# Optimization experiments

Hardware: AMD Instinct MI355X
Metric: run time of the kernel (lower is better)

Reference implementation:

```python
import jax, jax.numpy as jnp
import numpy as np

B, C, H, W = 8, 256, 132, 132
NH = 8          # num_head
WIN = 6         # pooled window (AdaptiveAvgPool2d output 6x6)


def setup_inputs() -> dict:
    key = jax.random.key(0)
    ks = jax.random.split(key, 16)
    def rn(k, shape, s=0.02):
        return jax.random.normal(k, shape, jnp.float32) * s
    d = {}
    d["x"] = jax.random.normal(ks[0], (B, C, H, W), jnp.float32)
    d["x_e"] = jax.random.normal(ks[1], (B, C, H, W), jnp.float32)
    # LayerNorms
    d["norm_w"] = jnp.ones((C,), jnp.float32); d["norm_b"] = jnp.zeros((C,), jnp.float32)
    d["norme_w"] = jnp.ones((C,), jnp.float32); d["norme_b"] = jnp.zeros((C,), jnp.float32)
    # GFA params (linears stored as (in, out))
    d["l_w"] = rn(ks[2], (C, C)); d["l_b"] = jnp.zeros((C,), jnp.float32)
    d["kv_w"] = rn(ks[3], (C, C)); d["kv_b"] = jnp.zeros((C,), jnp.float32)
    d["xe_w"] = rn(ks[4], (2 * C, C // 2)); d["xe_b"] = jnp.zeros((C // 2,), jnp.float32)
    # LFA params (single module, shared for both calls)
    d["q_w"] = rn(ks[5], (C, C // 2)); d["q_b"] = jnp.zeros((C // 2,), jnp.float32)
    d["ef_w"] = rn(ks[6], (C, C // 2)); d["ef_b"] = jnp.zeros((C // 2,), jnp.float32)
    d["ec_w"] = rn(ks[7], (C // 2, 1, 7, 7))   # depthwise 7x7, OIHW
    d["ec_b"] = jnp.zeros((C // 2,), jnp.float32)
    d["eb_w"] = rn(ks[8], (C // 2, C // 2)); d["eb_b"] = jnp.zeros((C // 2,), jnp.float32)
    # output projections (3C/2 -> C)
    d["proj_w"] = rn(ks[9], (3 * C // 2, C)); d["proj_b"] = jnp.zeros((C,), jnp.float32)
    d["proje_w"] = rn(ks[10], (3 * C // 2, C)); d["proje_b"] = jnp.zeros((C,), jnp.float32)
    return d


def _ln(x, w, b, eps=1e-6):
    m = x.mean(-1, keepdims=True)
    v = ((x - m) ** 2).mean(-1, keepdims=True)
    return (x - m) * jax.lax.rsqrt(v + eps) * w + b


def _gfa(x, xe, l_w, l_b, kv_w, kv_b, xe_w, xe_b):
    Bv, Hv, Wv, Cv = x.shape
    d = Cv // NH // 2                                   # per-head dim (=16)
    cat = jnp.concatenate([x, xe], -1)                  # (B,H,W,2C)
    xg = jax.nn.gelu(x @ l_w + l_b, approximate=False)  # nn.GELU exact
    kv = (xg @ kv_w + kv_b).reshape(Bv, Hv * Wv, 2, NH, d).transpose(2, 0, 3, 1, 4)
    k, v = kv[0], kv[1]                                 # (B,nh,HW,d)
    # AdaptiveAvgPool2d((6,6)) with H,W divisible by 6 == blocked mean
    pooled = cat.reshape(Bv, WIN, Hv // WIN, WIN, Wv // WIN, 2 * Cv).mean((2, 4))  # (B,6,6,2C)
    m = (pooled @ xe_w + xe_b).reshape(Bv, WIN * WIN, NH, d).transpose(0, 2, 1, 3)  # (B,nh,36,d)
    attn = jax.nn.softmax(jnp.einsum('bnqd,bnkd->bnqk', m * (d ** -0.5), k), axis=-1)
    out = jnp.einsum('bnqk,bnkd->bnqd', attn, v)        # (B,nh,36,d)
    out = out.reshape(Bv, NH, WIN, WIN, d).transpose(0, 1, 4, 2, 3).reshape(Bv, Cv // 2, WIN, WIN)
    up = jax.image.resize(out, (Bv, Cv // 2, Hv, Wv), 'bilinear')  # align_corners=False
    return up.transpose(0, 2, 3, 1)                     # (B,H,W,C/2)


def _lfa(x, xe, q_w, q_b, ef_w, ef_b, ec_w, ec_b, eb_w, eb_b):
    q = x @ q_w + q_b                                   # (B,H,W,C/2)
    e = (xe @ ef_w + ef_b).transpose(0, 3, 1, 2)        # (B,C/2,H,W)
    e = jax.lax.conv_general_dilated(
        e, ec_w, (1, 1), [(3, 3), (3, 3)],
        dimension_numbers=('NCHW', 'OIHW', 'NCHW'),
        feature_group_count=e.shape[1])
    e = (e + ec_b[None, :, None, None]).transpose(0, 2, 3, 1)
    e = e @ eb_w + eb_b
    return q * e


def reference(x, x_e, norm_w, norm_b, norme_w, norme_b,
              l_w, l_b, kv_w, kv_b, xe_w, xe_b,
              q_w, q_b, ef_w, ef_b, ec_w, ec_b, eb_w, eb_b,
              proj_w, proj_b, proje_w, proje_b):
    xc = x.transpose(0, 2, 3, 1)    # (B,H,W,C)
    xec = x_e.transpose(0, 2, 3, 1)
    xc = _ln(xc, norm_w, norm_b)
    xec = _ln(xec, norme_w, norme_b)
    g = _gfa(xc, xec, l_w, l_b, kv_w, kv_b, xe_w, xe_b)
    l1 = _lfa(xc, xec, q_w, q_b, ef_w, ef_b, ec_w, ec_b, eb_w, eb_b)
    l2 = _lfa(xec, xc, q_w, q_b, ef_w, ef_b, ec_w, ec_b, eb_w, eb_b)
    cat = jnp.concatenate([g, l1, l2], -1)              # (B,H,W,3C/2)
    out_e = (cat @ proje_w + proje_b).transpose(0, 3, 1, 2)
    out = (cat @ proj_w + proj_b).transpose(0, 3, 1, 2)
    return out, out_e
```

## Files before the change

### kernel.cpp

```cpp
#include <hip/hip_runtime.h>
#include <math.h>

#define HW_ 17424
#define WID 132
#define HGT 132
#define CH 256
#define MROWS 139392
#define OUTOFF 35684352

typedef __bf16 bf16x8 __attribute__((ext_vector_type(8)));
typedef float  f32x4  __attribute__((ext_vector_type(4)));

__device__ __forceinline__ void split8(const float* v, bf16x8& hi, bf16x8& lo) {
#pragma unroll
    for (int e = 0; e < 8; ++e) {
        float f = v[e];
        __bf16 h = (__bf16)f;
        hi[e] = h;
        lo[e] = (__bf16)(f - (float)h);
    }
}

__global__ __launch_bounds__(256)
void ln_k(const float* __restrict__ x, const float* __restrict__ w,
          const float* __restrict__ bias, float* __restrict__ out) {
    __shared__ float4 s1[256];
    __shared__ float4 s2[256];
    const int tid = threadIdx.x;
    const int b   = blockIdx.y;
    const int hw0 = blockIdx.x << 2;
    const float* px = x + ((size_t)(b * CH + tid)) * HW_ + hw0;
    float4 v = *(const float4*)px;
    s1[tid] = v;
    s2[tid] = make_float4(v.x * v.x, v.y * v.y, v.z * v.z, v.w * v.w);
    __syncthreads();
    for (int off = 128; off > 0; off >>= 1) {
        if (tid < off) {
            float4 a = s1[tid], c = s1[tid + off];
            a.x += c.x; a.y += c.y; a.z += c.z; a.w += c.w;
            s1[tid] = a;
            float4 d = s2[tid], e = s2[tid + off];
            d.x += e.x; d.y += e.y; d.z += e.z; d.w += e.w;
            s2[tid] = d;
        }
        __syncthreads();
    }
    float4 sum = s1[0], sq = s2[0];
    const float wv = w[tid], bv = bias[tid];
    const float inv = 1.0f / 256.0f;
    float o[4];
    {
        float m = sum.x * inv; float var = sq.x * inv - m * m;
        o[0] = (v.x - m) * rsqrtf(var + 1e-6f) * wv + bv;
    }
    {
        float m = sum.y * inv; float var = sq.y * inv - m * m;
        o[1] = (v.y - m) * rsqrtf(var + 1e-6f) * wv + bv;
    }
    {
        float m = sum.z * inv; float var = sq.z * inv - m * m;
        o[2] = (v.z - m) * rsqrtf(var + 1e-6f) * wv + bv;
    }
    {
        float m = sum.w * inv; float var = sq.w * inv - m * m;
        o[3] = (v.w - m) * rsqrtf(var + 1e-6f) * wv + bv;
    }
    float* po = out + ((size_t)(b * HW_ + hw0)) * CH + tid;
    po[0] = o[0]; po[256] = o[1]; po[512] = o[2]; po[768] = o[3];
}

template <int EPI, int KK, int NN>
__global__ __launch_bounds__(256, 2)
void mgemm_k(const float* __restrict__ A, const float* __restrict__ W,
             const float* __restrict__ bias, float* __restrict__ C,
             const float* __restrict__ mulbuf) {
    const int tid  = threadIdx.x;
    const int lane = tid & 63;
    const int wave = tid >> 6;
    const int wm = wave >> 1, wn = wave & 1;
    const int row0 = blockIdx.y * 128 + wm * 64;
    const int col0 = blockIdx.x * 128 + wn * 64;
    const int lrow = lane & 15;
    const int kg   = lane >> 4;

    const f32x4 zero = {0.f, 0.f, 0.f, 0.f};
    f32x4 acc[4][4];
#pragma unroll
    for (int i = 0; i < 4; ++i)
#pragma unroll
        for (int j = 0; j < 4; ++j) acc[i][j] = zero;

    for (int kt = 0; kt < KK; kt += 32) {
        const int kb = kt + kg * 8;
        bf16x8 ah[4], al[4], bh[4], bl[4];
#pragma unroll
        for (int mf = 0; mf < 4; ++mf) {
            const float* p = A + (size_t)(row0 + mf * 16 + lrow) * KK + kb;
            float buf[8];
            *(float4*)&buf[0] = *(const float4*)p;
            *(float4*)&buf[4] = *(const float4*)(p + 4);
            split8(buf, ah[mf], al[mf]);
        }
#pragma unroll
        for (int nf = 0; nf < 4; ++nf) {
            const float* p = W + (size_t)kb * NN + col0 + nf * 16 + lrow;
            float buf[8];
#pragma unroll
            for (int e = 0; e < 8; ++e) buf[e] = p[(size_t)e * NN];
            split8(buf, bh[nf], bl[nf]);
        }
#pragma unroll
        for (int mf = 0; mf < 4; ++mf)
#pragma unroll
            for (int nf = 0; nf < 4; ++nf) {
                f32x4 c = acc[mf][nf];
                c = __builtin_amdgcn_mfma_f32_16x16x32_bf16(al[mf], bh[nf], c, 0, 0, 0);
                c = __builtin_amdgcn_mfma_f32_16x16x32_bf16(ah[mf], bl[nf], c, 0, 0, 0);
                c = __builtin_amdgcn_mfma_f32_16x16x32_bf16(ah[mf], bh[nf], c, 0, 0, 0);
                acc[mf][nf] = c;
            }
    }

    float bv[4];
#pragma unroll
    for (int nf = 0; nf < 4; ++nf) bv[nf] = bias[col0 + nf * 16 + lrow];
#pragma unroll
    for (int mf = 0; mf < 4; ++mf) {
#pragma unroll
        for (int r = 0; r < 4; ++r) {
            const int row = row0 + mf * 16 + kg * 4 + r;
#pragma unroll
            for (int nf = 0; nf < 4; ++nf) {
                const int col = col0 + nf * 16 + lrow;
                const size_t off = (size_t)row * NN + col;
                float v = acc[mf][nf][r] + bv[nf];
                if (EPI == 1) v = 0.5f * v * (1.0f + erff(v * 0.7071067811865475f));
                if (EPI == 2) v *= mulbuf[off];
                C[off] = v;
            }
        }
    }
}

__global__ __launch_bounds__(256, 2)
void mgemm_proj_k(const float* __restrict__ g, const float* __restrict__ l1,
                  const float* __restrict__ l2,
                  const float* __restrict__ w1, const float* __restrict__ b1,
                  const float* __restrict__ w2, const float* __restrict__ b2,
                  float* __restrict__ out) {
    const int tid  = threadIdx.x;
    const int lane = tid & 63;
    const int wave = tid >> 6;
    const int wm = wave >> 1, wn = wave & 1;
    const int row0  = blockIdx.y * 128 + wm * 64;
    const int half  = blockIdx.x >> 1;
    const int ncol0 = (blockIdx.x & 1) * 128 + wn * 64;
    const float* Wsel = half ? w2 : w1;
    const float* bsel = half ? b2 : b1;
    float* obase = out + (half ? (size_t)OUTOFF : (size_t)0);
    const int lrow = lane & 15;
    const int kg   = lane >> 4;

    const f32x4 zero = {0.f, 0.f, 0.f, 0.f};
    f32x4 acc[4][4];
#pragma unroll
    for (int i = 0; i < 4; ++i)
#pragma unroll
        for (int j = 0; j < 4; ++j) acc[i][j] = zero;

    for (int kt = 0; kt < 384; kt += 32) {
        const float* Ab = (kt < 128) ? g : (kt < 256) ? l1 : l2;
        const int kloc = (kt & 127) + kg * 8;
        bf16x8 ah[4], al[4], bh[4], bl[4];
#pragma unroll
        for (int mf = 0; mf < 4; ++mf) {
            const float* p = Ab + (size_t)(row0 + mf * 16 + lrow) * 128 + kloc;
            float buf[8];
            *(float4*)&buf[0] = *(const float4*)p;
            *(float4*)&buf[4] = *(const float4*)(p + 4);
            split8(buf, ah[mf], al[mf]);
        }
#pragma unroll
        for (int nf = 0; nf < 4; ++nf) {
            const float* p = Wsel + (size_t)(kt + kg * 8) * 256 + ncol0 + nf * 16 + lrow;
            float buf[8];
#pragma unroll
            for (int e = 0; e < 8; ++e) buf[e] = p[(size_t)e * 256];
            split8(buf, bh[nf], bl[nf]);
        }
#pragma unroll
        for (int mf = 0; mf < 4; ++mf)
#pragma unroll
            for (int nf = 0; nf < 4; ++nf) {
                f32x4 c = acc[mf][nf];
                c = __builtin_amdgcn_mfma_f32_16x16x32_bf16(al[mf], bh[nf], c, 0, 0, 0);
                c = __builtin_amdgcn_mfma_f32_16x16x32_bf16(ah[mf], bl[nf], c, 0, 0, 0);
                c = __builtin_amdgcn_mfma_f32_16x16x32_bf16(ah[mf], bh[nf], c, 0, 0, 0);
                acc[mf][nf] = c;
            }
    }

    float bv[4];
#pragma unroll
    for (int nf = 0; nf < 4; ++nf) bv[nf] = bsel[ncol0 + nf * 16 + lrow];
#pragma unroll
    for (int mf = 0; mf < 4; ++mf) {
#pragma unroll
        for (int r = 0; r < 4; ++r) {
            const int row = row0 + mf * 16 + kg * 4 + r;
            const int bidx = row / HW_;
            const int hw = row - bidx * HW_;
#pragma unroll
            for (int nf = 0; nf < 4; ++nf) {
                const int c = ncol0 + nf * 16 + lrow;
                obase[((size_t)(bidx * 256 + c)) * HW_ + hw] = acc[mf][nf][r] + bv[nf];
            }
        }
    }
}

__global__ __launch_bounds__(256)
void pool_k(const float* __restrict__ xcl, const float* __restrict__ xel,
            float* __restrict__ pooled) {
    const int q = blockIdx.x;
    const int b = blockIdx.y;
    const int wi = q / 6, wj = q % 6;
    const int tid = threadIdx.x;
    const size_t base = ((size_t)(b * HW_ + wi * 22 * WID + wj * 22)) * CH + tid;
    const float* p0 = xcl + base;
    const float* p1 = xel + base;
    float s0 = 0.f, s1 = 0.f;
    for (int iy = 0; iy < 22; ++iy) {
        const size_t ro = (size_t)iy * WID * CH;
        for (int ix = 0; ix < 22; ++ix) {
            const size_t off = ro + (size_t)ix * CH;
            s0 += p0[off];
            s1 += p1[off];
        }
    }
    const float inv = 1.0f / 484.0f;
    float* dst = pooled + (size_t)(b * 36 + q) * 512;
    dst[tid] = s0 * inv;
    dst[256 + tid] = s1 * inv;
}

__global__ __launch_bounds__(128)
void mproj_k(const float* __restrict__ pooled, const float* __restrict__ xe_w,
             const float* __restrict__ xe_b, float* __restrict__ mbuf) {
    __shared__ float p[512];
    const int q = blockIdx.x, b = blockIdx.y, tid = threadIdx.x;
    const float* prow = pooled + (size_t)(b * 36 + q) * 512;
    for (int i = tid; i < 512; i += 128) p[i] = prow[i];
    __syncthreads();
    float acc = xe_b[tid];
    for (int k = 0; k < 512; ++k) acc += p[k] * xe_w[k * 128 + tid];
    mbuf[(size_t)(b * 36 + q) * 128 + tid] = acc;
}

__global__ __launch_bounds__(256)
void attn_k(const float* __restrict__ mbuf, const float* __restrict__ kv,
            float* __restrict__ aout) {
    const int qg = blockIdx.x;
    const int head = blockIdx.y, b = blockIdx.z;
    const int tid = threadIdx.x;
    __shared__ float ml[6][16];
    if (tid < 96) {
        const int q = tid >> 4, d = tid & 15;
        ml[q][d] = mbuf[(size_t)(b * 36 + qg * 6 + q) * 128 + head * 16 + d];
    }
    __syncthreads();

    float mx[6], sum[6], a[6][16];
#pragma unroll
    for (int q = 0; q < 6; ++q) {
        mx[q] = -INFINITY; sum[q] = 0.f;
#pragma unroll
        for (int d = 0; d < 16; ++d) a[q][d] = 0.f;
    }

    for (int j = tid; j < HW_; j += 256) {
        const float* row = kv + ((size_t)(b * HW_ + j)) * 256 + head * 16;
        float k[16], v[16];
        *(float4*)&k[0]  = *(const float4*)(row + 0);
        *(float4*)&k[4]  = *(const float4*)(row + 4);
        *(float4*)&k[8]  = *(const float4*)(row + 8);
        *(float4*)&k[12] = *(const float4*)(row + 12);
        const float* vr = row + 128;
        *(float4*)&v[0]  = *(const float4*)(vr + 0);
        *(float4*)&v[4]  = *(const float4*)(vr + 4);
        *(float4*)&v[8]  = *(const float4*)(vr + 8);
        *(float4*)&v[12] = *(const float4*)(vr + 12);
#pragma unroll
        for (int q = 0; q < 6; ++q) {
            float s = 0.f;
#pragma unroll
            for (int d = 0; d < 16; ++d) s += ml[q][d] * k[d];
            s *= 0.25f;
            const float nm = fmaxf(mx[q], s);
            const float corr = expf(mx[q] - nm);
            const float p = expf(s - nm);
            sum[q] = sum[q] * corr + p;
#pragma unroll
            for (int d = 0; d < 16; ++d) a[q][d] = a[q][d] * corr + p * v[d];
            mx[q] = nm;
        }
    }

    __shared__ float smax[256];
    __shared__ float ssum[256];
    __shared__ float sacc[256][16];
    for (int q = 0; q < 6; ++q) {
        __syncthreads();
        smax[tid] = mx[q]; ssum[tid] = sum[q];
#pragma unroll
        for (int d = 0; d < 16; ++d) sacc[tid][d] = a[q][d];
        for (int off = 128; off > 0; off >>= 1) {
            __syncthreads();
            if (tid < off) {
                const float ma = smax[tid], mb = smax[tid + off];
                const float nm = fmaxf(ma, mb);
                const float ea = expf(ma - nm), eb = expf(mb - nm);
                ssum[tid] = ssum[tid] * ea + ssum[tid + off] * eb;
                for (int d = 0; d < 16; ++d)
                    sacc[tid][d] = sacc[tid][d] * ea + sacc[tid + off][d] * eb;
                smax[tid] = nm;
            }
        }
        __syncthreads();
        if (tid < 16)
            aout[((size_t)(b * 8 + head) * 36 + qg * 6 + q) * 16 + tid] =
                sacc[0][tid] / ssum[0];
    }
}

__global__ __launch_bounds__(256)
void upsample_k(const float* __restrict__ aout, float* __restrict__ g) {
    const int tid = threadIdx.x;
    const int c = tid & 127;
    const int hw = blockIdx.x * 2 + (tid >> 7);
    const int b = blockIdx.y;
    const int h = hw / WID;
    const int w = hw - h * WID;
    const float fy = (h - 10.5f) * (1.0f / 22.0f);
    const float fx = (w - 10.5f) * (1.0f / 22.0f);
    float y0f = floorf(fy), x0f = floorf(fx);
    const float ty = fy - y0f, tx = fx - x0f;
    int y0 = (int)y0f, x0 = (int)x0f;
    int y1 = min(y0 + 1, 5), x1 = min(x0 + 1, 5);
    y0 = max(y0, 0); x0 = max(x0, 0);
    const int head = c >> 4, di = c & 15;
    const float* src = aout + ((size_t)(b * 8 + head) * 36) * 16 + di;
    const float s00 = src[(y0 * 6 + x0) * 16];
    const float s01 = src[(y0 * 6 + x1) * 16];
    const float s10 = src[(y1 * 6 + x0) * 16];
    const float s11 = src[(y1 * 6 + x1) * 16];
    const float v = (1.f - ty) * ((1.f - tx) * s00 + tx * s01)
                  + ty * ((1.f - tx) * s10 + tx * s11);
    g[((size_t)(b * HW_ + hw)) * 128 + c] = v;
}

__global__ __launch_bounds__(256)
void dwconv_k(const float* __restrict__ in, const float* __restrict__ cw,
              const float* __restrict__ cb, float* __restrict__ out) {
    __shared__ float wl[128 * 49];
    const int tid = threadIdx.x;
    for (int i = tid; i < 128 * 49; i += 256) wl[i] = cw[i];
    __syncthreads();
    const int c  = tid & 127;
    const int xb = ((blockIdx.x << 1) + (tid >> 7)) * 22;
    const int h  = blockIdx.y;
    const int b  = blockIdx.z;
    const float* wc = &wl[c * 49];
    float acc[22];
    const float bias = cb[c];
#pragma unroll
    for (int i = 0; i < 22; ++i) acc[i] = bias;
    const float* ibase = in + ((size_t)b * HW_) * 128 + c;
    for (int ky = 0; ky < 7; ++ky) {
        const int y = h + ky - 3;
        if ((unsigned)y >= (unsigned)HGT) continue;
        const float* rp = ibase + (size_t)y * WID * 128;
        float v[28];
#pragma unroll
        for (int j = 0; j < 28; ++j) {
            const int x = xb - 3 + j;
            v[j] = ((unsigned)x < (unsigned)WID) ? rp[(size_t)x * 128] : 0.f;
        }
#pragma unroll
        for (int kx = 0; kx < 7; ++kx) {
            const float wv = wc[ky * 7 + kx];
#pragma unroll
            for (int i = 0; i < 22; ++i) acc[i] += v[i + kx] * wv;
        }
    }
    float* op = out + ((size_t)(b * HW_ + h * WID + xb)) * 128 + c;
#pragma unroll
    for (int i = 0; i < 22; ++i) op[(size_t)i * 128] = acc[i];
}

extern "C" void kernel_launch(void* const* d_in, const int* in_sizes, int n_in,
                              void* d_out, int out_size, void* d_ws, size_t ws_size,
                              hipStream_t stream) {
    const float* x      = (const float*)d_in[0];
    const float* x_e    = (const float*)d_in[1];
    const float* norm_w = (const float*)d_in[2];
    const float* norm_b = (const float*)d_in[3];
    const float* norme_w= (const float*)d_in[4];
    const float* norme_b= (const float*)d_in[5];
    const float* l_w    = (const float*)d_in[6];
    const float* l_b    = (const float*)d_in[7];
    const float* kv_w   = (const float*)d_in[8];
    const float* kv_b   = (const float*)d_in[9];
    const float* xe_w   = (const float*)d_in[10];
    const float* xe_b   = (const float*)d_in[11];
    const float* q_w    = (const float*)d_in[12];
    const float* q_b    = (const float*)d_in[13];
    const float* ef_w   = (const float*)d_in[14];
    const float* ef_b   = (const float*)d_in[15];
    const float* ec_w   = (const float*)d_in[16];
    const float* ec_b   = (const float*)d_in[17];
    const float* eb_w   = (const float*)d_in[18];
    const float* eb_b   = (const float*)d_in[19];
    const float* proj_w = (const float*)d_in[20];
    const float* proj_b = (const float*)d_in[21];
    const float* proje_w= (const float*)d_in[22];
    const float* proje_b= (const float*)d_in[23];
    float* out = (float*)d_out;

    float* ws = (float*)d_ws;
    const size_t MS = (size_t)MROWS * 256;
    const size_t MH = (size_t)MROWS * 128;
    float* P0 = ws;
    float* P1 = ws + MS;
    float* P2 = ws + 2 * MS;
    float* P3 = ws + 3 * MS;
    float* pooled = ws + 4 * MS;
    float* mbuf = pooled + 147456;
    float* aout = mbuf + 36864;
    float* P2a = P2;
    float* P2b = P2 + MH;
    float* P3a = P3;
    float* P3b = P3 + MH;

    const dim3 blk(256);
    ln_k<<<dim3(HW_ / 4, 8), blk, 0, stream>>>(x, norm_w, norm_b, P0);
    ln_k<<<dim3(HW_ / 4, 8), blk, 0, stream>>>(x_e, norme_w, norme_b, P1);
    mgemm_k<1, 256, 256><<<dim3(2, MROWS / 128), blk, 0, stream>>>(P0, l_w, l_b, P2, nullptr);
    mgemm_k<0, 256, 256><<<dim3(2, MROWS / 128), blk, 0, stream>>>(P2, kv_w, kv_b, P3, nullptr);
    pool_k<<<dim3(36, 8), blk, 0, stream>>>(P0, P1, pooled);
    mproj_k<<<dim3(36, 8), dim3(128), 0, stream>>>(pooled, xe_w, xe_b, mbuf);
    attn_k<<<dim3(6, 8, 8), blk, 0, stream>>>(mbuf, P3, aout);
    mgemm_k<0, 256, 128><<<dim3(1, MROWS / 128), blk, 0, stream>>>(P1, ef_w, ef_b, P2a, nullptr);
    dwconv_k<<<dim3(3, HGT, 8), blk, 0, stream>>>(P2a, ec_w, ec_b, P2b);
    mgemm_k<0, 256, 128><<<dim3(1, MROWS / 128), blk, 0, stream>>>(P0, q_w, q_b, P3a, nullptr);
    mgemm_k<2, 128, 128><<<dim3(1, MROWS / 128), blk, 0, stream>>>(P2b, eb_w, eb_b, P3a, P3a);
    mgemm_k<0, 256, 128><<<dim3(1, MROWS / 128), blk, 0, stream>>>(P0, ef_w, ef_b, P2a, nullptr);
    dwconv_k<<<dim3(3, HGT, 8), blk, 0, stream>>>(P2a, ec_w, ec_b, P2b);
    mgemm_k<0, 256, 128><<<dim3(1, MROWS / 128), blk, 0, stream>>>(P1, q_w, q_b, P3b, nullptr);
    mgemm_k<2, 128, 128><<<dim3(1, MROWS / 128), blk, 0, stream>>>(P2b, eb_w, eb_b, P3b, P3b);
    upsample_k<<<dim3(HW_ / 2, 8), blk, 0, stream>>>(aout, P2a);
    mgemm_proj_k<<<dim3(4, MROWS / 128), blk, 0, stream>>>(
        P2a, P3a, P3b, proj_w, proj_b, proje_w, proje_b, out);
}
```

Baseline: 2.488 ms.

## Pre-split weights to transposed bf16 hi/lo and fuse q/ef projection GEMMs

Adds a prep kernel that converts each weight matrix once per call into transposed bf16 hi/lo arrays. The GEMMs can then load contiguous 8-element vectors instead of doing strided scalar fp32 loads and splitting in every tile. It also merges the q and ef projections that share an input into one GEMM with N=256, so each LayerNorm output is read once instead of twice, and reorders the LFA launches and buffers so P0 is reused for the dwconv output. The cost is several extra small launches and extra workspace for the converted weights.

```diff
diff --git a/kernel.cpp b/kernel.cpp
--- a/kernel.cpp
+++ b/kernel.cpp
@@ -10,6 +10,7 @@
 
 typedef __bf16 bf16x8 __attribute__((ext_vector_type(8)));
 typedef float  f32x4  __attribute__((ext_vector_type(4)));
+typedef unsigned short ushort_t;
 
 __device__ __forceinline__ void split8(const float* v, bf16x8& hi, bf16x8& lo) {
 #pragma unroll
@@ -19,6 +20,20 @@
         hi[e] = h;
         lo[e] = (__bf16)(f - (float)h);
     }
+}
+
+__global__ __launch_bounds__(256)
+void prep_w_k(const float* __restrict__ W, ushort_t* __restrict__ hi,
+              ushort_t* __restrict__ lo, int K, int N, int coloff, int KT) {
+    const int idx = blockIdx.x * 256 + threadIdx.x;
+    if (idx >= K * N) return;
+    const int n = idx / K, k = idx - n * K;
+    const float f = W[(size_t)k * N + n];
+    const __bf16 h = (__bf16)f;
+    const __bf16 l = (__bf16)(f - (float)h);
+    const size_t d = (size_t)(coloff + n) * KT + k;
+    hi[d] = __builtin_bit_cast(ushort_t, h);
+    lo[d] = __builtin_bit_cast(ushort_t, l);
 }
 
 __global__ __launch_bounds__(256)
@@ -71,9 +86,9 @@
 
 template <int EPI, int KK, int NN>
 __global__ __launch_bounds__(256, 2)
-void mgemm_k(const float* __restrict__ A, const float* __restrict__ W,
-             const float* __restrict__ bias, float* __restrict__ C,
-             const float* __restrict__ mulbuf) {
+void mgemm_k(const float* __restrict__ A, const ushort_t* __restrict__ Whi,
+             const ushort_t* __restrict__ Wlo, const float* __restrict__ bias,
+             float* __restrict__ C, const float* __restrict__ mulbuf) {
     const int tid  = threadIdx.x;
     const int lane = tid & 63;
     const int wave = tid >> 6;
@@ -94,20 +109,18 @@
         const int kb = kt + kg * 8;
         bf16x8 ah[4], al[4], bh[4], bl[4];
 #pragma unroll
+        for (int nf = 0; nf < 4; ++nf) {
+            const size_t wo = (size_t)(col0 + nf * 16 + lrow) * KK + kb;
+            bh[nf] = *(const bf16x8*)(Whi + wo);
+            bl[nf] = *(const bf16x8*)(Wlo + wo);
+        }
+#pragma unroll
         for (int mf = 0; mf < 4; ++mf) {
             const float* p = A + (size_t)(row0 + mf * 16 + lrow) * KK + kb;
             float buf[8];
             *(float4*)&buf[0] = *(const float4*)p;
             *(float4*)&buf[4] = *(const float4*)(p + 4);
             split8(buf, ah[mf], al[mf]);
-        }
-#pragma unroll
-        for (int nf = 0; nf < 4; ++nf) {
-            const float* p = W + (size_t)kb * NN + col0 + nf * 16 + lrow;
-            float buf[8];
-#pragma unroll
-            for (int e = 0; e < 8; ++e) buf[e] = p[(size_t)e * NN];
-            split8(buf, bh[nf], bl[nf]);
         }
 #pragma unroll
         for (int mf = 0; mf < 4; ++mf)
@@ -143,19 +156,84 @@
 }
 
 __global__ __launch_bounds__(256, 2)
+void mgemm_dual_k(const float* __restrict__ A, const ushort_t* __restrict__ Whi,
+                  const ushort_t* __restrict__ Wlo, const float* __restrict__ qb,
+                  const float* __restrict__ efb, float* __restrict__ Cq,
+                  float* __restrict__ Ce) {
+    const int tid  = threadIdx.x;
+    const int lane = tid & 63;
+    const int wave = tid >> 6;
+    const int wm = wave >> 1, wn = wave & 1;
+    const int row0 = blockIdx.y * 128 + wm * 64;
+    const int col0 = blockIdx.x * 128 + wn * 64;
+    const int lrow = lane & 15;
+    const int kg   = lane >> 4;
+
+    const f32x4 zero = {0.f, 0.f, 0.f, 0.f};
+    f32x4 acc[4][4];
+#pragma unroll
+    for (int i = 0; i < 4; ++i)
+#pragma unroll
+        for (int j = 0; j < 4; ++j) acc[i][j] = zero;
+
+    for (int kt = 0; kt < 256; kt += 32) {
+        const int kb = kt + kg * 8;
+        bf16x8 ah[4], al[4], bh[4], bl[4];
+#pragma unroll
+        for (int nf = 0; nf < 4; ++nf) {
+            const size_t wo = (size_t)(col0 + nf * 16 + lrow) * 256 + kb;
+            bh[nf] = *(const bf16x8*)(Whi + wo);
+            bl[nf] = *(const bf16x8*)(Wlo + wo);
+        }
+#pragma unroll
+        for (int mf = 0; mf < 4; ++mf) {
+            const float* p = A + (size_t)(row0 + mf * 16 + lrow) * 256 + kb;
+            float buf[8];
+            *(float4*)&buf[0] = *(const float4*)p;
+            *(float4*)&buf[4] = *(const float4*)(p + 4);
+            split8(buf, ah[mf], al[mf]);
+        }
+#pragma unroll
+        for (int mf = 0; mf < 4; ++mf)
+#pragma unroll
+            for (int nf = 0; nf < 4; ++nf) {
+                f32x4 c = acc[mf][nf];
+                c = __builtin_amdgcn_mfma_f32_16x16x32_bf16(al[mf], bh[nf], c, 0, 0, 0);
+                c = __builtin_amdgcn_mfma_f32_16x16x32_bf16(ah[mf], bl[nf], c, 0, 0, 0);
+                c = __builtin_amdgcn_mfma_f32_16x16x32_bf16(ah[mf], bh[nf], c, 0, 0, 0);
+                acc[mf][nf] = c;
+            }
+    }
+
+#pragma unroll
+    for (int nf = 0; nf < 4; ++nf) {
+        const int col = col0 + nf * 16 + lrow;
+        const float bv = (col < 128) ? qb[col] : efb[col - 128];
+        float* base = (col < 128) ? Cq : Ce;
+        const int cl = col & 127;
+#pragma unroll
+        for (int mf = 0; mf < 4; ++mf)
+#pragma unroll
+            for (int r = 0; r < 4; ++r) {
+                const int row = row0 + mf * 16 + kg * 4 + r;
+                base[(size_t)row * 128 + cl] = acc[mf][nf][r] + bv;
+            }
+    }
+}
+
+__global__ __launch_bounds__(256, 2)
 void mgemm_proj_k(const float* __restrict__ g, const float* __restrict__ l1,
                   const float* __restrict__ l2,
-                  const float* __restrict__ w1, const float* __restrict__ b1,
-                  const float* __restrict__ w2, const float* __restrict__ b2,
+                  const ushort_t* __restrict__ Whi, const ushort_t* __restrict__ Wlo,
+                  const float* __restrict__ b1, const float* __restrict__ b2,
                   float* __restrict__ out) {
     const int tid  = threadIdx.x;
     const int lane = tid & 63;
     const int wave = tid >> 6;
     const int wm = wave >> 1, wn = wave & 1;
-    const int row0  = blockIdx.y * 128 + wm * 64;
-    const int half  = blockIdx.x >> 1;
-    const int ncol0 = (blockIdx.x & 1) * 128 + wn * 64;
-    const float* Wsel = half ? w2 : w1;
+    const int row0 = blockIdx.y * 128 + wm * 64;
+    const int col0 = blockIdx.x * 128 + wn * 64;
+    const int half = col0 >> 8;
     const float* bsel = half ? b2 : b1;
     float* obase = out + (half ? (size_t)OUTOFF : (size_t)0);
     const int lrow = lane & 15;
@@ -171,7 +249,14 @@
     for (int kt = 0; kt < 384; kt += 32) {
         const float* Ab = (kt < 128) ? g : (kt < 256) ? l1 : l2;
         const int kloc = (kt & 127) + kg * 8;
+        const int kb = kt + kg * 8;
         bf16x8 ah[4], al[4], bh[4], bl[4];
+#pragma unroll
+        for (int nf = 0; nf < 4; ++nf) {
+            const size_t wo = (size_t)(col0 + nf * 16 + lrow) * 384 + kb;
+            bh[nf] = *(const bf16x8*)(Whi + wo);
+            bl[nf] = *(const bf16x8*)(Wlo + wo);
+        }
 #pragma unroll
         for (int mf = 0; mf < 4; ++mf) {
             const float* p = Ab + (size_t)(row0 + mf * 16 + lrow) * 128 + kloc;
@@ -181,14 +266,6 @@
             split8(buf, ah[mf], al[mf]);
         }
 #pragma unroll
-        for (int nf = 0; nf < 4; ++nf) {
-            const float* p = Wsel + (size_t)(kt + kg * 8) * 256 + ncol0 + nf * 16 + lrow;
-            float buf[8];
-#pragma unroll
-            for (int e = 0; e < 8; ++e) buf[e] = p[(size_t)e * 256];
-            split8(buf, bh[nf], bl[nf]);
-        }
-#pragma unroll
         for (int mf = 0; mf < 4; ++mf)
 #pragma unroll
             for (int nf = 0; nf < 4; ++nf) {
@@ -202,7 +279,7 @@
 
     float bv[4];
 #pragma unroll
-    for (int nf = 0; nf < 4; ++nf) bv[nf] = bsel[ncol0 + nf * 16 + lrow];
+    for (int nf = 0; nf < 4; ++nf) bv[nf] = bsel[(col0 & 255) + nf * 16 + lrow];
 #pragma unroll
     for (int mf = 0; mf < 4; ++mf) {
 #pragma unroll
@@ -212,7 +289,7 @@
             const int hw = row - bidx * HW_;
 #pragma unroll
             for (int nf = 0; nf < 4; ++nf) {
-                const int c = ncol0 + nf * 16 + lrow;
+                const int c = (col0 & 255) + nf * 16 + lrow;
                 obase[((size_t)(bidx * 256 + c)) * HW_ + hw] = acc[mf][nf][r] + bv[nf];
             }
         }
@@ -437,28 +514,47 @@
     float* pooled = ws + 4 * MS;
     float* mbuf = pooled + 147456;
     float* aout = mbuf + 36864;
+    float* P0a = P0;
+    float* P0b = P0 + MH;
     float* P2a = P2;
     float* P2b = P2 + MH;
     float* P3a = P3;
     float* P3b = P3 + MH;
 
+    ushort_t* wsp = (ushort_t*)(aout + 36864);
+    ushort_t* Wl_hi  = wsp;
+    ushort_t* Wl_lo  = Wl_hi  + 65536;
+    ushort_t* Wkv_hi = Wl_lo  + 65536;
+    ushort_t* Wkv_lo = Wkv_hi + 65536;
+    ushort_t* Wqe_hi = Wkv_lo + 65536;
+    ushort_t* Wqe_lo = Wqe_hi + 65536;
+    ushort_t* Web_hi = Wqe_lo + 65536;
+    ushort_t* Web_lo = Web_hi + 16384;
+    ushort_t* Wp_hi  = Web_lo + 16384;
+    ushort_t* Wp_lo  = Wp_hi  + 196608;
+
     const dim3 blk(256);
+    prep_w_k<<<dim3(256), blk, 0, stream>>>(l_w,    Wl_hi,  Wl_lo,  256, 256, 0,   256);
+    prep_w_k<<<dim3(256), blk, 0, stream>>>(kv_w,   Wkv_hi, Wkv_lo, 256, 256, 0,   256);
+    prep_w_k<<<dim3(128), blk, 0, stream>>>(q_w,    Wqe_hi, Wqe_lo, 256, 128, 0,   256);
+    prep_w_k<<<dim3(128), blk, 0, stream>>>(ef_w,   Wqe_hi, Wqe_lo, 256, 128, 128, 256);
+    prep_w_k<<<dim3(64),  blk, 0, stream>>>(eb_w,   Web_hi, Web_lo, 128, 128, 0,   128);
+    prep_w_k<<<dim3(384), blk, 0, stream>>>(proj_w, Wp_hi,  Wp_lo,  384, 256, 0,   384);
+    prep_w_k<<<dim3(384), blk, 0, stream>>>(proje_w,Wp_hi,  Wp_lo,  384, 256, 256, 384);
     ln_k<<<dim3(HW_ / 4, 8), blk, 0, stream>>>(x, norm_w, norm_b, P0);
     ln_k<<<dim3(HW_ / 4, 8), blk, 0, stream>>>(x_e, norme_w, norme_b, P1);
-    mgemm_k<1, 256, 256><<<dim3(2, MROWS / 128), blk, 0, stream>>>(P0, l_w, l_b, P2, nullptr);
-    mgemm_k<0, 256, 256><<<dim3(2, MROWS / 128), blk, 0, stream>>>(P2, kv_w, kv_b, P3, nullptr);
+    mgemm_k<1, 256, 256><<<dim3(2, MROWS / 128), blk, 0, stream>>>(P0, Wl_hi, Wl_lo, l_b, P2, nullptr);
+    mgemm_k<0, 256, 256><<<dim3(2, MROWS / 128), blk, 0, stream>>>(P2, Wkv_hi, Wkv_lo, kv_b, P3, nullptr);
     pool_k<<<dim3(36, 8), blk, 0, stream>>>(P0, P1, pooled);
     mproj_k<<<dim3(36, 8), dim3(128), 0, stream>>>(pooled, xe_w, xe_b, mbuf);
     attn_k<<<dim3(6, 8, 8), blk, 0, stream>>>(mbuf, P3, aout);
-    mgemm_k<0, 256, 128><<<dim3(1, MROWS / 128), blk, 0, stream>>>(P1, ef_w, ef_b, P2a, nullptr);
-    dwconv_k<<<dim3(3, HGT, 8), blk, 0, stream>>>(P2a, ec_w, ec_b, P2b);
-    mgemm_k<0, 256, 128><<<dim3(1, MROWS / 128), blk, 0, stream>>>(P0, q_w, q_b, P3a, nullptr);
-    mgemm_k<2, 128, 128><<<dim3(1, MROWS / 128), blk, 0, stream>>>(P2b, eb_w, eb_b, P3a, P3a);
-    mgemm_k<0, 256, 128><<<dim3(1, MROWS / 128), blk, 0, stream>>>(P0, ef_w, ef_b, P2a, nullptr);
-    dwconv_k<<<dim3(3, HGT, 8), blk, 0, stream>>>(P2a, ec_w, ec_b, P2b);
-    mgemm_k<0, 256, 128><<<dim3(1, MROWS / 128), blk, 0, stream>>>(P1, q_w, q_b, P3b, nullptr);
-    mgemm_k<2, 128, 128><<<dim3(1, MROWS / 128), blk, 0, stream>>>(P2b, eb_w, eb_b, P3b, P3b);
+    mgemm_dual_k<<<dim3(2, MROWS / 128), blk, 0, stream>>>(P0, Wqe_hi, Wqe_lo, q_b, ef_b, P3a, P2a);
+    mgemm_dual_k<<<dim3(2, MROWS / 128), blk, 0, stream>>>(P1, Wqe_hi, Wqe_lo, q_b, ef_b, P3b, P2b);
+    dwconv_k<<<dim3(3, HGT, 8), blk, 0, stream>>>(P2a, ec_w, ec_b, P0a);
+    dwconv_k<<<dim3(3, HGT, 8), blk, 0, stream>>>(P2b, ec_w, ec_b, P0b);
+    mgemm_k<2, 128, 128><<<dim3(1, MROWS / 128), blk, 0, stream>>>(P0b, Web_hi, Web_lo, eb_b, P3a, P3a);
+    mgemm_k<2, 128, 128><<<dim3(1, MROWS / 128), blk, 0, stream>>>(P0a, Web_hi, Web_lo, eb_b, P3b, P3b);
     upsample_k<<<dim3(HW_ / 2, 8), blk, 0, stream>>>(aout, P2a);
     mgemm_proj_k<<<dim3(4, MROWS / 128), blk, 0, stream>>>(
-        P2a, P3a, P3b, proj_w, proj_b, proje_w, proje_b, out);
-}
+        P2a, P3a, P3b, Wp_hi, Wp_lo, proj_b, proje_b, out);
+}
```

New measurement: 2.593 ms. 1.04x slower.
